# Optimization experiments

Measured on AMD Instinct MI355X. Metric: run time of the kernel, lower is better.

Reference implementation:

```python
import jax, jax.numpy as jnp
import numpy as np

NUM_HEADS = 12
H = W = 64            # spatial grid (SAM ViT-B global attention)
DIM = 768
HEAD_DIM = DIM // NUM_HEADS


def setup_inputs() -> dict:
    key = jax.random.key(0)
    ks = jax.random.split(key, 7)
    return {
        "x": jax.random.normal(ks[0], (1, H, W, DIM), dtype=jnp.float32),
        "qkv_w": jax.random.normal(ks[1], (3 * DIM, DIM), dtype=jnp.float32) * 0.02,
        "qkv_b": jax.random.normal(ks[2], (3 * DIM,), dtype=jnp.float32) * 0.02,
        "proj_w": jax.random.normal(ks[3], (DIM, DIM), dtype=jnp.float32) * 0.02,
        "proj_b": jax.random.normal(ks[4], (DIM,), dtype=jnp.float32) * 0.02,
        "rel_pos_h": jax.random.normal(ks[5], (2 * H - 1, HEAD_DIM), dtype=jnp.float32) * 0.02,
        "rel_pos_w": jax.random.normal(ks[6], (2 * W - 1, HEAD_DIM), dtype=jnp.float32) * 0.02,
    }


def _get_rel_pos(size: int, rel_pos: jnp.ndarray) -> jnp.ndarray:
    # q_size == k_size == size; rel_pos already has length 2*size-1 (no interp).
    coords = jnp.arange(size)[:, None] - jnp.arange(size)[None, :] + (size - 1)
    return rel_pos[coords]  # [size, size, head_dim]


def reference(x, qkv_w, qkv_b, proj_w, proj_b, rel_pos_h, rel_pos_w):
    B, h, w, C = x.shape
    nh, hd = NUM_HEADS, C // NUM_HEADS
    S = h * w
    scale = hd ** -0.5

    qkv = x.reshape(B, S, C) @ qkv_w.T + qkv_b            # [B, S, 3C]
    qkv = qkv.reshape(B, S, 3, nh, hd).transpose(2, 0, 3, 1, 4)
    qkv = qkv.reshape(3, B * nh, S, hd)
    q, k, v = qkv[0], qkv[1], qkv[2]                      # [B*nh, S, hd]

    attn = jnp.einsum('bqc,bkc->bqk', q * scale, k)       # [B*nh, S, S]

    Rh = _get_rel_pos(h, rel_pos_h)                       # [h, h, hd]
    Rw = _get_rel_pos(w, rel_pos_w)                       # [w, w, hd]
    r_q = q.reshape(B * nh, h, w, hd)
    rel_h = jnp.einsum('bhwc,hkc->bhwk', r_q, Rh)         # [B*nh, h, w, h]
    rel_w = jnp.einsum('bhwc,wkc->bhwk', r_q, Rw)         # [B*nh, h, w, w]
    attn = (attn.reshape(B * nh, h, w, h, w)
            + rel_h[:, :, :, :, None]
            + rel_w[:, :, :, None, :]).reshape(B * nh, S, S)

    attn = jax.nn.softmax(attn, axis=-1)
    out = jnp.einsum('bqk,bkc->bqc', attn, v)             # [B*nh, S, hd]
    out = out.reshape(B, nh, h, w, hd).transpose(0, 2, 3, 1, 4).reshape(B, h, w, C)
    return out @ proj_w.T + proj_b
```

## Files before the change

kernel.cpp:

```cpp
#include <hip/hip_runtime.h>


typedef __bf16 bf16;
typedef __bf16 bf16x8 __attribute__((ext_vector_type(8)));
typedef __bf16 bf16x4 __attribute__((ext_vector_type(4)));
typedef float f32x4 __attribute__((ext_vector_type(4)));

__device__ __forceinline__ f32x4 mfma16(bf16x8 a, bf16x8 b, f32x4 c) {
  return __builtin_amdgcn_mfma_f32_16x16x32_bf16(a, b, c, 0, 0, 0);
}

typedef const __attribute__((address_space(1))) void* gas_ptr;
typedef __attribute__((address_space(3))) void* las_ptr;
__device__ __forceinline__ void gl_lds16(const void* g, void* l) {
  __builtin_amdgcn_global_load_lds((gas_ptr)g, (las_ptr)l, 16, 0, 0);
}

#define L2E 1.4426950408889634f

__global__ __launch_bounds__(256) void cvt3(
    const float* __restrict__ a, bf16* __restrict__ oa,
    const float* __restrict__ b, bf16* __restrict__ ob,
    const float* __restrict__ c, bf16* __restrict__ oc) {
  int blk = blockIdx.x;
  const float* src;
  bf16* dst;
  int base;
  if (blk < 1536)       { src = a; dst = oa; base = blk; }
  else if (blk < 2400)  { src = b; dst = ob; base = blk - 1536; }
  else                  { src = c; dst = oc; base = blk - 2400; }
  int idx = (base * 256 + threadIdx.x) * 8;
  f32x4 x = *(const f32x4*)&src[idx];
  f32x4 y = *(const f32x4*)&src[idx + 4];
  bf16x8 o;
#pragma unroll
  for (int j = 0; j < 4; j++) { o[j] = (bf16)x[j]; o[j + 4] = (bf16)y[j]; }
  *(bf16x8*)&dst[idx] = o;
}

template <int MODE>
__global__ __launch_bounds__(256) void gemm128(
    const bf16* __restrict__ A, const bf16* __restrict__ B,
    const float* __restrict__ bias, int K, int N,
    bf16* __restrict__ q_s, bf16* __restrict__ k_s, bf16* __restrict__ v_t,
    float* __restrict__ outf) {
  __shared__ __align__(16) bf16 lA[128 * 32];
  __shared__ __align__(16) bf16 lB[128 * 32];
  const int tid = threadIdx.x;
  const int w = tid >> 6, l = tid & 63;
  const int n0 = blockIdx.x * 128, m0 = blockIdx.y * 128;

  f32x4 acc[4][4] = {};

  const int ch0 = w * 2, ch1 = ch0 + 1;
  const int r0 = ch0 * 16 + (l >> 2), r1 = ch1 * 16 + (l >> 2);
  const int ce = (l & 3) * 8;
  const int mw = (w & 1) * 64, nw = (w >> 1) * 64;

  for (int k0 = 0; k0 < K; k0 += 32) {
    __syncthreads();
    gl_lds16(&A[(size_t)(m0 + r0) * K + k0 + ce], &lA[ch0 * 512]);
    gl_lds16(&A[(size_t)(m0 + r1) * K + k0 + ce], &lA[ch1 * 512]);
    gl_lds16(&B[(size_t)(n0 + r0) * K + k0 + ce], &lB[ch0 * 512]);
    gl_lds16(&B[(size_t)(n0 + r1) * K + k0 + ce], &lB[ch1 * 512]);
    __syncthreads();
    bf16x8 af[4], bfr[4];
#pragma unroll
    for (int i = 0; i < 4; i++)
      af[i] = *(const bf16x8*)&lA[(mw + i * 16 + (l & 15)) * 32 + (l >> 4) * 8];
#pragma unroll
    for (int i = 0; i < 4; i++)
      bfr[i] = *(const bf16x8*)&lB[(nw + i * 16 + (l & 15)) * 32 + (l >> 4) * 8];
#pragma unroll
    for (int mi = 0; mi < 4; mi++)
#pragma unroll
      for (int ni = 0; ni < 4; ni++)
        acc[mi][ni] = mfma16(af[mi], bfr[ni], acc[mi][ni]);
  }

#pragma unroll
  for (int ni = 0; ni < 4; ni++) {
    const int n = n0 + nw + ni * 16 + (l & 15);
    const float bv = bias[n];
#pragma unroll
    for (int mi = 0; mi < 4; mi++) {
#pragma unroll
      for (int i = 0; i < 4; i++) {
        const int m = m0 + mw + mi * 16 + (l >> 4) * 4 + i;
        const float v = acc[mi][ni][i] + bv;
        if (MODE == 0) {
          const int which = n / 768, hn = n % 768;
          const int head = hn >> 6, hd = hn & 63;
          if (which == 0)      q_s[((size_t)head * 4096 + m) * 64 + hd] = (bf16)v;
          else if (which == 1) k_s[((size_t)head * 4096 + m) * 64 + hd] = (bf16)v;
          else                 v_t[((size_t)head * 64 + hd) * 4096 + m] = (bf16)v;
        } else {
          outf[(size_t)m * N + n] = v;
        }
      }
    }
  }
}

__global__ __launch_bounds__(64) void rel_pos_w(
    const bf16* __restrict__ q_s, const float* __restrict__ table,
    float* __restrict__ out) {
  const int l = threadIdx.x;
  const int p = blockIdx.x, head = blockIdx.y;
  const size_t hbase = (size_t)head * 4096 * 64;

  f32x4 acc[4][4] = {};
#pragma unroll
  for (int ks = 0; ks < 2; ks++) {
    bf16x8 af[4], bfr[4];
#pragma unroll
    for (int mi = 0; mi < 4; mi++) {
      const int row = mi * 16 + (l & 15);
      const int s = row * 64 + p;
      af[mi] = *(const bf16x8*)&q_s[hbase + (size_t)s * 64 + ks * 32 + (l >> 4) * 8];
    }
#pragma unroll
    for (int ni = 0; ni < 4; ni++) {
      const int col = ni * 16 + (l & 15);
      const float* tp = &table[(size_t)(p - col + 63) * 64 + ks * 32 + (l >> 4) * 8];
      f32x4 t0 = *(const f32x4*)tp;
      f32x4 t1 = *(const f32x4*)(tp + 4);
      bf16x8 bb;
#pragma unroll
      for (int j = 0; j < 4; j++) { bb[j] = (bf16)t0[j]; bb[j + 4] = (bf16)t1[j]; }
      bfr[ni] = bb;
    }
#pragma unroll
    for (int mi = 0; mi < 4; mi++)
#pragma unroll
      for (int ni = 0; ni < 4; ni++)
        acc[mi][ni] = mfma16(af[mi], bfr[ni], acc[mi][ni]);
  }
#pragma unroll
  for (int mi = 0; mi < 4; mi++)
#pragma unroll
    for (int ni = 0; ni < 4; ni++)
#pragma unroll
      for (int i = 0; i < 4; i++) {
        const int row = mi * 16 + (l >> 4) * 4 + i;
        const int col = ni * 16 + (l & 15);
        const int sq = row * 64 + p;
        out[hbase + (size_t)sq * 64 + col] = acc[mi][ni][i];
      }
}

__global__ __launch_bounds__(256) void flash_attn(
    const bf16* __restrict__ q_s, const bf16* __restrict__ k_s,
    const bf16* __restrict__ v_t, const float* __restrict__ rph,
    const float* __restrict__ bias_w, bf16* __restrict__ attn_out) {
  __shared__ __align__(16) bf16 lK[2][64 * 64];
  __shared__ __align__(16) bf16 lV[2][64 * 64];
  __shared__ float lBH[64 * 65];

  const int tid = threadIdx.x;
  const int w = tid >> 6, l = tid & 63;
  const int g = l >> 4, q16 = l & 15;
  const int qh = blockIdx.x, head = blockIdx.y;
  const size_t hbase = (size_t)head * 4096 * 64;
  const int qloc = w * 16 + q16;
  const size_t sq = (size_t)qh * 64 + qloc;

  bf16x8 qf[2];
  qf[0] = *(const bf16x8*)&q_s[hbase + sq * 64 + g * 8];
  qf[1] = *(const bf16x8*)&q_s[hbase + sq * 64 + 32 + g * 8];

  const int cb = l & 7;
  const int ch0 = w * 2, ch1 = ch0 + 1;
  const int rk0 = ch0 * 8 + (l >> 3), rk1 = ch1 * 8 + (l >> 3);
  const int fk0 = ((rk0 >> 3) & 3) * 2 + (rk0 & 1);
  const int fk1 = ((rk1 >> 3) & 3) * 2 + (rk1 & 1);
  const int skc0 = (cb ^ fk0) * 8, skc1 = (cb ^ fk1) * 8;
  const int svc0 = (cb ^ (rk0 & 7)) * 8, svc1 = (cb ^ (rk1 & 7)) * 8;

#define STAGE(buf, t)                                                          \
  do {                                                                         \
    gl_lds16(&k_s[hbase + (size_t)((t) * 64 + rk0) * 64 + skc0],               \
             &lK[buf][ch0 * 512]);                                             \
    gl_lds16(&k_s[hbase + (size_t)((t) * 64 + rk1) * 64 + skc1],               \
             &lK[buf][ch1 * 512]);                                             \
    gl_lds16(&v_t[hbase + (size_t)rk0 * 4096 + (t) * 64 + svc0],               \
             &lV[buf][ch0 * 512]);                                             \
    gl_lds16(&v_t[hbase + (size_t)rk1 * 4096 + (t) * 64 + svc1],               \
             &lV[buf][ch1 * 512]);                                             \
  } while (0)

  STAGE(0, 0);

  {
    f32x4 abh[4] = {};
#pragma unroll
    for (int ks = 0; ks < 2; ks++)
#pragma unroll
      for (int ni = 0; ni < 4; ni++) {
        const int t = ni * 16 + q16;
        const float* tp = &rph[(size_t)(qh + 63 - t) * 64 + ks * 32 + g * 8];
        f32x4 t0 = *(const f32x4*)tp;
        f32x4 t1 = *(const f32x4*)(tp + 4);
        bf16x8 rf;
#pragma unroll
        for (int j = 0; j < 4; j++) { rf[j] = (bf16)t0[j]; rf[j + 4] = (bf16)t1[j]; }
        abh[ni] = mfma16(rf, qf[ks], abh[ni]);
      }
#pragma unroll
    for (int ni = 0; ni < 4; ni++)
#pragma unroll
      for (int i = 0; i < 4; i++)
        lBH[qloc * 65 + ni * 16 + g * 4 + i] = abh[ni][i];
  }

  float c2[4][4];
#pragma unroll
  for (int ni = 0; ni < 4; ni++)
#pragma unroll
    for (int i = 0; i < 4; i++) {
      const int kw = (ni >> 1) * 32 + g * 8 + (ni & 1) * 4 + i;
      c2[ni][i] = bias_w[hbase + sq * 64 + kw] * L2E;
    }

  f32x4 oacc[4] = {};
  float mrun = -1e30f, lrun = 0.f;
  const float SC2 = 0.125f * L2E;

  __syncthreads();

  int cur = 0;
  for (int t = 0; t < 64; t++) {
    STAGE(cur ^ 1, (t + 1 < 64) ? t + 1 : 63);

    f32x4 sa[4] = {};
#pragma unroll
    for (int ks = 0; ks < 2; ks++)
#pragma unroll
      for (int ni = 0; ni < 4; ni++) {
        const int key =
            (ni >> 1) * 32 + ((l & 15) >> 2) * 8 + (ni & 1) * 4 + (l & 3);
        const int fk = ((key >> 3) & 3) * 2 + (key & 1);
        bf16x8 kf =
            *(const bf16x8*)&lK[cur][key * 64 + ((ks * 4 + g) ^ fk) * 8];
        sa[ni] = mfma16(kf, qf[ks], sa[ni]);
      }

    const float bh2 = lBH[qloc * 65 + t] * L2E;
    float p[4][4];
    float smax = -1e30f;
#pragma unroll
    for (int ni = 0; ni < 4; ni++)
#pragma unroll
      for (int i = 0; i < 4; i++) {
        p[ni][i] = sa[ni][i] * SC2 + c2[ni][i];
        smax = fmaxf(smax, p[ni][i]);
      }
    smax = fmaxf(smax, __shfl_xor(smax, 16, 64));
    smax = fmaxf(smax, __shfl_xor(smax, 32, 64));
    const float rmf = smax + bh2;

    if (!__all(rmf - mrun <= 8.f)) {
      const float mn = fmaxf(mrun, rmf);
      const float al = __builtin_amdgcn_exp2f(mrun - mn);
      mrun = mn;
      lrun *= al;
#pragma unroll
      for (int nh = 0; nh < 4; nh++)
#pragma unroll
        for (int i = 0; i < 4; i++) oacc[nh][i] *= al;
    }

    const float d = bh2 - mrun;
    float rs = 0.f;
#pragma unroll
    for (int ni = 0; ni < 4; ni++)
#pragma unroll
      for (int i = 0; i < 4; i++) {
        p[ni][i] = __builtin_amdgcn_exp2f(p[ni][i] + d);
        rs += p[ni][i];
      }
    rs += __shfl_xor(rs, 16, 64);
    rs += __shfl_xor(rs, 32, 64);
    lrun += rs;

    bf16x8 pb[2];
#pragma unroll
    for (int ks = 0; ks < 2; ks++)
#pragma unroll
      for (int j = 0; j < 8; j++)
        pb[ks][j] = (bf16)p[2 * ks + (j >> 2)][j & 3];

#pragma unroll
    for (int ks = 0; ks < 2; ks++)
#pragma unroll
      for (int nh = 0; nh < 4; nh++) {
        const int hd = nh * 16 + q16;
        bf16x8 vf =
            *(const bf16x8*)&lV[cur][hd * 64 + ((ks * 4 + g) ^ (hd & 7)) * 8];
        oacc[nh] = mfma16(vf, pb[ks], oacc[nh]);
      }

    __syncthreads();
    cur ^= 1;
  }
#undef STAGE

  const float inv = 1.0f / lrun;
#pragma unroll
  for (int nh = 0; nh < 4; nh++) {
    bf16x4 ov;
#pragma unroll
    for (int i = 0; i < 4; i++) ov[i] = (bf16)(oacc[nh][i] * inv);
    *(bf16x4*)&attn_out[sq * 768 + head * 64 + nh * 16 + g * 4] = ov;
  }
}

extern "C" void kernel_launch(void* const* d_in, const int* in_sizes, int n_in,
                              void* d_out, int out_size, void* d_ws, size_t ws_size,
                              hipStream_t stream) {
  const float* x      = (const float*)d_in[0];
  const float* qkv_w  = (const float*)d_in[1];
  const float* qkv_b  = (const float*)d_in[2];
  const float* proj_w = (const float*)d_in[3];
  const float* proj_b = (const float*)d_in[4];
  const float* rph    = (const float*)d_in[5];
  const float* rpw    = (const float*)d_in[6];

  char* ws = (char*)d_ws;
  bf16*  xb    = (bf16*)(ws);
  bf16*  wqkv  = (bf16*)(ws + 6291456);
  bf16*  wproj = (bf16*)(ws + 9830400);
  bf16*  q_s   = (bf16*)(ws + 11010048);
  bf16*  k_s   = (bf16*)(ws + 17301504);
  bf16*  v_t   = (bf16*)(ws + 23592960);
  bf16*  attno = (bf16*)(ws + 29884416);
  float* bwv   = (float*)(ws + 36175872);

  cvt3<<<2688, 256, 0, stream>>>(x, xb, qkv_w, wqkv, proj_w, wproj);

  gemm128<0><<<dim3(18, 32), 256, 0, stream>>>(xb, wqkv, qkv_b, 768, 2304,
                                               q_s, k_s, v_t, nullptr);

  rel_pos_w<<<dim3(64, 12), 64, 0, stream>>>(q_s, rpw, bwv);

  flash_attn<<<dim3(64, 12), 256, 0, stream>>>(q_s, k_s, v_t, rph, bwv, attno);

  gemm128<1><<<dim3(6, 32), 256, 0, stream>>>(attno, wproj, proj_b, 768, 768,
                                              nullptr, nullptr, nullptr,
                                              (float*)d_out);
}
```

Before: 257.3 us.

## Use 32x32 MFMA with split-key waves and merge partial softmax states

Moves the flash attention inner loop from 16x16x32 to 32x32x16 bf16 MFMA. Each wave now handles 32 queries against half of each 64-key tile, so two waves share a query group. Their online-softmax states are merged through LDS at the end. Per-tile pointer increments replace recomputed staging addresses, the K swizzle is simplified, and the P operand is rebuilt with cross-half shuffles instead of a register repack. This aims for higher MFMA throughput and fewer LDS reads per FLOP, at the cost of extra shuffles, an end-of-kernel reduction and more registers.

```diff
diff --git a/kernel.cpp b/kernel.cpp
--- a/kernel.cpp
+++ b/kernel.cpp
@@ -5,9 +5,14 @@
 typedef __bf16 bf16x8 __attribute__((ext_vector_type(8)));
 typedef __bf16 bf16x4 __attribute__((ext_vector_type(4)));
 typedef float f32x4 __attribute__((ext_vector_type(4)));
+typedef float f32x16 __attribute__((ext_vector_type(16)));
+typedef unsigned int u32;
 
 __device__ __forceinline__ f32x4 mfma16(bf16x8 a, bf16x8 b, f32x4 c) {
   return __builtin_amdgcn_mfma_f32_16x16x32_bf16(a, b, c, 0, 0, 0);
+}
+__device__ __forceinline__ f32x16 mfma32(bf16x8 a, bf16x8 b, f32x16 c) {
+  return __builtin_amdgcn_mfma_f32_32x32x16_bf16(a, b, c, 0, 0, 0);
 }
 
 typedef const __attribute__((address_space(1))) void* gas_ptr;
@@ -153,76 +158,91 @@
     const bf16* __restrict__ q_s, const bf16* __restrict__ k_s,
     const bf16* __restrict__ v_t, const float* __restrict__ rph,
     const float* __restrict__ bias_w, bf16* __restrict__ attn_out) {
-  __shared__ __align__(16) bf16 lK[2][64 * 64];
-  __shared__ __align__(16) bf16 lV[2][64 * 64];
-  __shared__ float lBH[64 * 65];
+  __shared__ __align__(16) char smem[49408];
+  bf16* lKb = (bf16*)smem;
+  bf16* lVb = (bf16*)(smem + 16384);
+  float* lBH = (float*)(smem + 32768);
 
   const int tid = threadIdx.x;
   const int w = tid >> 6, l = tid & 63;
-  const int g = l >> 4, q16 = l & 15;
+  const int r5 = l & 31, h = l >> 5, r7 = l & 7;
+  const int qg = w & 1, kh2 = w >> 1;
   const int qh = blockIdx.x, head = blockIdx.y;
-  const size_t hbase = (size_t)head * 4096 * 64;
-  const int qloc = w * 16 + q16;
+  const size_t hbase = (size_t)head << 18;
+  const int qloc = qg * 32 + r5;
   const size_t sq = (size_t)qh * 64 + qloc;
 
-  bf16x8 qf[2];
-  qf[0] = *(const bf16x8*)&q_s[hbase + sq * 64 + g * 8];
-  qf[1] = *(const bf16x8*)&q_s[hbase + sq * 64 + 32 + g * 8];
-
-  const int cb = l & 7;
   const int ch0 = w * 2, ch1 = ch0 + 1;
-  const int rk0 = ch0 * 8 + (l >> 3), rk1 = ch1 * 8 + (l >> 3);
-  const int fk0 = ((rk0 >> 3) & 3) * 2 + (rk0 & 1);
-  const int fk1 = ((rk1 >> 3) & 3) * 2 + (rk1 & 1);
-  const int skc0 = (cb ^ fk0) * 8, skc1 = (cb ^ fk1) * 8;
-  const int svc0 = (cb ^ (rk0 & 7)) * 8, svc1 = (cb ^ (rk1 & 7)) * 8;
-
-#define STAGE(buf, t)                                                          \
-  do {                                                                         \
-    gl_lds16(&k_s[hbase + (size_t)((t) * 64 + rk0) * 64 + skc0],               \
-             &lK[buf][ch0 * 512]);                                             \
-    gl_lds16(&k_s[hbase + (size_t)((t) * 64 + rk1) * 64 + skc1],               \
-             &lK[buf][ch1 * 512]);                                             \
-    gl_lds16(&v_t[hbase + (size_t)rk0 * 4096 + (t) * 64 + svc0],               \
-             &lV[buf][ch0 * 512]);                                             \
-    gl_lds16(&v_t[hbase + (size_t)rk1 * 4096 + (t) * 64 + svc1],               \
-             &lV[buf][ch1 * 512]);                                             \
+  const int lr3 = l >> 3;
+  const int swz = ((l & 7) ^ lr3) * 8;
+  const bf16* kp0 = k_s + hbase + (size_t)(ch0 * 8 + lr3) * 64 + swz;
+  const bf16* kp1 = k_s + hbase + (size_t)(ch1 * 8 + lr3) * 64 + swz;
+  const bf16* vp0 = v_t + hbase + (size_t)(ch0 * 8 + lr3) * 4096 + swz;
+  const bf16* vp1 = v_t + hbase + (size_t)(ch1 * 8 + lr3) * 4096 + swz;
+
+#define STAGE(buf)                                                        \
+  do {                                                                    \
+    gl_lds16(kp0, smem + (buf) * 8192 + ch0 * 1024);                      \
+    gl_lds16(kp1, smem + (buf) * 8192 + ch1 * 1024);                      \
+    gl_lds16(vp0, smem + 16384 + (buf) * 8192 + ch0 * 1024);              \
+    gl_lds16(vp1, smem + 16384 + (buf) * 8192 + ch1 * 1024);              \
   } while (0)
 
-  STAGE(0, 0);
+  STAGE(0);
+  kp0 += 4096; kp1 += 4096; vp0 += 64; vp1 += 64;
 
   {
+    const int q16 = l & 15, g4 = l >> 4;
+    const size_t sq16 = (size_t)qh * 64 + w * 16 + q16;
+    bf16x8 qf16[2];
+    qf16[0] = *(const bf16x8*)&q_s[hbase + sq16 * 64 + g4 * 8];
+    qf16[1] = *(const bf16x8*)&q_s[hbase + sq16 * 64 + 32 + g4 * 8];
     f32x4 abh[4] = {};
 #pragma unroll
     for (int ks = 0; ks < 2; ks++)
 #pragma unroll
       for (int ni = 0; ni < 4; ni++) {
-        const int t = ni * 16 + q16;
-        const float* tp = &rph[(size_t)(qh + 63 - t) * 64 + ks * 32 + g * 8];
+        const int kh = ni * 16 + q16;
+        const float* tp = &rph[(size_t)(qh + 63 - kh) * 64 + ks * 32 + g4 * 8];
         f32x4 t0 = *(const f32x4*)tp;
         f32x4 t1 = *(const f32x4*)(tp + 4);
         bf16x8 rf;
 #pragma unroll
         for (int j = 0; j < 4; j++) { rf[j] = (bf16)t0[j]; rf[j + 4] = (bf16)t1[j]; }
-        abh[ni] = mfma16(rf, qf[ks], abh[ni]);
+        abh[ni] = mfma16(rf, qf16[ks], abh[ni]);
       }
 #pragma unroll
     for (int ni = 0; ni < 4; ni++)
 #pragma unroll
       for (int i = 0; i < 4; i++)
-        lBH[qloc * 65 + ni * 16 + g * 4 + i] = abh[ni][i];
-  }
-
-  float c2[4][4];
-#pragma unroll
-  for (int ni = 0; ni < 4; ni++)
-#pragma unroll
-    for (int i = 0; i < 4; i++) {
-      const int kw = (ni >> 1) * 32 + g * 8 + (ni & 1) * 4 + i;
-      c2[ni][i] = bias_w[hbase + sq * 64 + kw] * L2E;
-    }
-
-  f32x4 oacc[4] = {};
+        lBH[(w * 16 + q16) * 65 + ni * 16 + g4 * 4 + i] = abh[ni][i];
+  }
+
+  bf16x8 qv[4];
+#pragma unroll
+  for (int s = 0; s < 4; s++)
+    qv[s] = *(const bf16x8*)&q_s[hbase + sq * 64 + s * 16 + h * 8];
+
+  float c2[16];
+#pragma unroll
+  for (int G = 0; G < 4; G++) {
+    f32x4 cv = *(const f32x4*)&bias_w[hbase + sq * 64 + kh2 * 32 + G * 8 + h * 4];
+#pragma unroll
+    for (int i = 0; i < 4; i++) c2[G * 4 + i] = cv[i] * L2E;
+  }
+
+  int offK[4], offV[2][2];
+  const int rowK = kh2 * 32 + r5;
+#pragma unroll
+  for (int s = 0; s < 4; s++)
+    offK[s] = rowK * 128 + (((s * 2 + h) ^ r7) * 16);
+#pragma unroll
+  for (int T = 0; T < 2; T++)
+#pragma unroll
+    for (int st = 0; st < 2; st++)
+      offV[T][st] = (T * 32 + r5) * 128 + (((kh2 * 4 + st * 2 + h) ^ r7) * 16);
+
+  f32x16 o[2] = {};
   float mrun = -1e30f, lrun = 0.f;
   const float SC2 = 0.125f * L2E;
 
@@ -230,88 +250,112 @@
 
   int cur = 0;
   for (int t = 0; t < 64; t++) {
-    STAGE(cur ^ 1, (t + 1 < 64) ? t + 1 : 63);
-
-    f32x4 sa[4] = {};
-#pragma unroll
-    for (int ks = 0; ks < 2; ks++)
-#pragma unroll
-      for (int ni = 0; ni < 4; ni++) {
-        const int key =
-            (ni >> 1) * 32 + ((l & 15) >> 2) * 8 + (ni & 1) * 4 + (l & 3);
-        const int fk = ((key >> 3) & 3) * 2 + (key & 1);
-        bf16x8 kf =
-            *(const bf16x8*)&lK[cur][key * 64 + ((ks * 4 + g) ^ fk) * 8];
-        sa[ni] = mfma16(kf, qf[ks], sa[ni]);
-      }
-
+    if (t < 63) {
+      STAGE(cur ^ 1);
+      kp0 += 4096; kp1 += 4096; vp0 += 64; vp1 += 64;
+    }
+
+    const char* kb = smem + cur * 8192;
+    f32x16 sacc = {0.f, 0.f, 0.f, 0.f, 0.f, 0.f, 0.f, 0.f,
+                   0.f, 0.f, 0.f, 0.f, 0.f, 0.f, 0.f, 0.f};
+#pragma unroll
+    for (int s = 0; s < 4; s++) {
+      bf16x8 kf = *(const bf16x8*)(kb + offK[s]);
+      sacc = mfma32(kf, qv[s], sacc);
+    }
+
+    float p[16], pm = -1e30f;
+#pragma unroll
+    for (int j = 0; j < 16; j++) {
+      p[j] = sacc[j] * SC2 + c2[j];
+      pm = fmaxf(pm, p[j]);
+    }
+    pm = fmaxf(pm, __shfl_xor(pm, 32, 64));
     const float bh2 = lBH[qloc * 65 + t] * L2E;
-    float p[4][4];
-    float smax = -1e30f;
-#pragma unroll
-    for (int ni = 0; ni < 4; ni++)
-#pragma unroll
-      for (int i = 0; i < 4; i++) {
-        p[ni][i] = sa[ni][i] * SC2 + c2[ni][i];
-        smax = fmaxf(smax, p[ni][i]);
-      }
-    smax = fmaxf(smax, __shfl_xor(smax, 16, 64));
-    smax = fmaxf(smax, __shfl_xor(smax, 32, 64));
-    const float rmf = smax + bh2;
+    const float rmf = pm + bh2;
 
     if (!__all(rmf - mrun <= 8.f)) {
       const float mn = fmaxf(mrun, rmf);
       const float al = __builtin_amdgcn_exp2f(mrun - mn);
       mrun = mn;
       lrun *= al;
-#pragma unroll
-      for (int nh = 0; nh < 4; nh++)
-#pragma unroll
-        for (int i = 0; i < 4; i++) oacc[nh][i] *= al;
+      o[0] *= al;
+      o[1] *= al;
     }
 
     const float d = bh2 - mrun;
     float rs = 0.f;
-#pragma unroll
-    for (int ni = 0; ni < 4; ni++)
-#pragma unroll
-      for (int i = 0; i < 4; i++) {
-        p[ni][i] = __builtin_amdgcn_exp2f(p[ni][i] + d);
-        rs += p[ni][i];
-      }
-    rs += __shfl_xor(rs, 16, 64);
+    u32 w8[8];
+#pragma unroll
+    for (int j = 0; j < 8; j++) {
+      float e0 = __builtin_amdgcn_exp2f(p[2 * j] + d);
+      float e1 = __builtin_amdgcn_exp2f(p[2 * j + 1] + d);
+      rs += e0 + e1;
+      union { bf16 b[2]; u32 u; } cvu;
+      cvu.b[0] = (bf16)e0;
+      cvu.b[1] = (bf16)e1;
+      w8[j] = cvu.u;
+    }
     rs += __shfl_xor(rs, 32, 64);
     lrun += rs;
 
-    bf16x8 pb[2];
-#pragma unroll
-    for (int ks = 0; ks < 2; ks++)
-#pragma unroll
-      for (int j = 0; j < 8; j++)
-        pb[ks][j] = (bf16)p[2 * ks + (j >> 2)][j & 3];
-
-#pragma unroll
-    for (int ks = 0; ks < 2; ks++)
-#pragma unroll
-      for (int nh = 0; nh < 4; nh++) {
-        const int hd = nh * 16 + q16;
-        bf16x8 vf =
-            *(const bf16x8*)&lV[cur][hd * 64 + ((ks * 4 + g) ^ (hd & 7)) * 8];
-        oacc[nh] = mfma16(vf, pb[ks], oacc[nh]);
-      }
+    const char* vb = smem + 16384 + cur * 8192;
+#pragma unroll
+    for (int st = 0; st < 2; st++) {
+      u32 x0 = h ? w8[4 * st] : w8[4 * st + 2];
+      u32 x1 = h ? w8[4 * st + 1] : w8[4 * st + 3];
+      u32 p0 = (u32)__shfl_xor((int)x0, 32, 64);
+      u32 p1 = (u32)__shfl_xor((int)x1, 32, 64);
+      union { u32 u[4]; bf16x8 v; } pf;
+      pf.u[0] = h ? p0 : w8[4 * st];
+      pf.u[1] = h ? p1 : w8[4 * st + 1];
+      pf.u[2] = h ? w8[4 * st + 2] : p0;
+      pf.u[3] = h ? w8[4 * st + 3] : p1;
+#pragma unroll
+      for (int T = 0; T < 2; T++) {
+        bf16x8 vf = *(const bf16x8*)(vb + offV[T][st]);
+        o[T] = mfma32(vf, pf.v, o[T]);
+      }
+    }
 
     __syncthreads();
     cur ^= 1;
   }
 #undef STAGE
 
-  const float inv = 1.0f / lrun;
-#pragma unroll
-  for (int nh = 0; nh < 4; nh++) {
-    bf16x4 ov;
-#pragma unroll
-    for (int i = 0; i < 4; i++) ov[i] = (bf16)(oacc[nh][i] * inv);
-    *(bf16x4*)&attn_out[sq * 768 + head * 64 + nh * 16 + g * 4] = ov;
+  float* MM = (float*)smem;
+  float* ML = (float*)(smem + 256);
+  float* MO = (float*)(smem + 512);
+  if (w >= 2) {
+    if (h == 0) { MM[qg * 32 + r5] = mrun; ML[qg * 32 + r5] = lrun; }
+#pragma unroll
+    for (int T = 0; T < 2; T++)
+#pragma unroll
+      for (int G = 0; G < 4; G++) {
+        f32x4 ov;
+#pragma unroll
+        for (int i = 0; i < 4; i++) ov[i] = o[T][4 * G + i];
+        *(f32x4*)&MO[qg * 2048 + r5 * 64 + T * 32 + G * 8 + h * 4] = ov;
+      }
+  }
+  __syncthreads();
+  if (w < 2) {
+    const float mp = MM[qg * 32 + r5], lp = ML[qg * 32 + r5];
+    const float mT = fmaxf(mrun, mp);
+    const float a = __builtin_amdgcn_exp2f(mrun - mT);
+    const float b = __builtin_amdgcn_exp2f(mp - mT);
+    const float inv = 1.f / (lrun * a + lp * b);
+#pragma unroll
+    for (int T = 0; T < 2; T++)
+#pragma unroll
+      for (int G = 0; G < 4; G++) {
+        f32x4 po = *(const f32x4*)&MO[qg * 2048 + r5 * 64 + T * 32 + G * 8 + h * 4];
+        bf16x4 ob;
+#pragma unroll
+        for (int i = 0; i < 4; i++)
+          ob[i] = (bf16)((o[T][4 * G + i] * a + po[i] * b) * inv);
+        *(bf16x4*)&attn_out[sq * 768 + head * 64 + T * 32 + G * 8 + h * 4] = ob;
+      }
   }
 }
 
```

New measurement: 306.3 us. 1.19x slower.
